# Kernel tuning notes

Hardware: AMD Instinct MI355X
Metric: run time of the kernel (lower is better)

## Reference

```python
import jax, jax.numpy as jnp
import numpy as np

D_MODEL = 1024
NUM_HEADS = 16
HEAD_DIM = D_MODEL // NUM_HEADS
NUM_KERNELS = 21


def tisa_bias(amp, off, sharp, seq_len):
    # amp/off/sharp: (H, K). Returns (H, L, L) translation-invariant bias.
    # Evaluate on the 2L-1 distinct relative distances, then gather (Toeplitz).
    d = jnp.arange(-(seq_len - 1), seq_len, dtype=amp.dtype)  # (2L-1,)
    # (H, K, 2L-1) -> sum over kernels -> (H, 2L-1)
    scores = jnp.sum(
        amp[:, :, None]
        * jnp.exp(-jnp.abs(sharp)[:, :, None] * (d[None, None, :] - off[:, :, None]) ** 2),
        axis=1,
    )
    i = jnp.arange(seq_len)
    rel_idx = i[None, :] - i[:, None] + (seq_len - 1)  # (L, L) in [0, 2L-2]
    return scores[:, rel_idx]  # (H, L, L)


def setup_inputs() -> dict:
    key = jax.random.key(0)
    ks = jax.random.split(key, 9)
    B, L = 4, 1024
    s = 0.02
    return {
        "x_q": jax.random.normal(ks[0], (B, L, D_MODEL), dtype=jnp.float32),
        "x_kv": jax.random.normal(ks[1], (B, L, D_MODEL), dtype=jnp.float32),
        "Wq": jax.random.normal(ks[2], (D_MODEL, D_MODEL), dtype=jnp.float32) * s,
        "Wm": jax.random.normal(ks[3], (D_MODEL, 2 * D_MODEL), dtype=jnp.float32) * s,
        "Wg": jax.random.normal(ks[4], (D_MODEL, 2 * D_MODEL), dtype=jnp.float32) * s,
        "bg": jnp.zeros((2 * D_MODEL,), dtype=jnp.float32),
        "tisa_amp": jax.random.normal(ks[5], (NUM_HEADS, NUM_KERNELS), dtype=jnp.float32) * 0.1,
        "tisa_off": jax.random.uniform(ks[6], (NUM_HEADS, NUM_KERNELS), dtype=jnp.float32, minval=-512.0, maxval=512.0),
        "tisa_sharp": jax.random.uniform(ks[7], (NUM_HEADS, NUM_KERNELS), dtype=jnp.float32, minval=1e-4, maxval=0.05),
    }


def reference(x_q, x_kv, Wq, Wm, Wg, bg, tisa_amp, tisa_off, tisa_sharp):
    B, Lq, _ = x_q.shape
    Lkv = x_kv.shape[1]
    H, Dh = NUM_HEADS, HEAD_DIM

    q = (x_q @ Wq).reshape(B, Lq, H, Dh).transpose(0, 2, 1, 3)        # (B,H,Lq,Dh)
    mem = (x_kv @ Wm)                                                 # (B,Lkv,2D)
    k = mem[..., :D_MODEL].reshape(B, Lkv, H, Dh).transpose(0, 2, 1, 3)
    v = mem[..., D_MODEL:].reshape(B, Lkv, H, Dh).transpose(0, 2, 1, 3)

    scale = 1.0 / jnp.sqrt(jnp.asarray(Dh, dtype=q.dtype))
    scores = jnp.einsum("bhqd,bhkd->bhqk", q, k) * scale              # (B,H,Lq,Lkv)
    scores = scores + tisa_bias(tisa_amp, tisa_off, tisa_sharp, Lkv)[None]
    weights = jax.nn.softmax(scores, axis=-1)

    attn = jnp.einsum("bhqk,bhkd->bhqd", weights, v)                  # (B,H,Lq,Dh)
    attn = attn.transpose(0, 2, 1, 3).reshape(B, Lq, D_MODEL)

    g = attn @ Wg + bg                                                # (B,Lq,2D)
    a, b = g[..., :D_MODEL], g[..., D_MODEL:]
    return a * jax.nn.sigmoid(b)
```

## Files before the change

### kernel.cpp

```cpp
#include <hip/hip_runtime.h>
#include <cstdint>
#include <cstddef>

typedef __attribute__((ext_vector_type(8))) short bf16x8;
typedef __attribute__((ext_vector_type(4))) float f32x4;

#define LOG2E 1.44269504f

__device__ __forceinline__ unsigned short f2bf(float x) {
  unsigned int u = __float_as_uint(x);
  u += 0x7FFFu + ((u >> 16) & 1u);
  return (unsigned short)(u >> 16);
}
__device__ __forceinline__ unsigned short f2bf_trunc(float x) {
  return (unsigned short)(__float_as_uint(x) >> 16);
}

__device__ __forceinline__ bf16x8 pack8(const float4& a, const float4& b) {
  bf16x8 r;
  r[0] = (short)f2bf(a.x); r[1] = (short)f2bf(a.y);
  r[2] = (short)f2bf(a.z); r[3] = (short)f2bf(a.w);
  r[4] = (short)f2bf(b.x); r[5] = (short)f2bf(b.y);
  r[6] = (short)f2bf(b.z); r[7] = (short)f2bf(b.w);
  return r;
}

__device__ __forceinline__ void gload_lds16(const void* g, void* l) {
  __builtin_amdgcn_global_load_lds(
      (const __attribute__((address_space(1))) unsigned int*)g,
      (__attribute__((address_space(3))) unsigned int*)l, 16, 0, 0);
}


__global__ void preproc(const float* __restrict__ Wq, const float* __restrict__ Wm,
                        const float* __restrict__ Wg,
                        const float* __restrict__ amp, const float* __restrict__ off,
                        const float* __restrict__ sharp,
                        unsigned short* __restrict__ dWq, unsigned short* __restrict__ dWm,
                        unsigned short* __restrict__ dWg, float* __restrict__ tab) {
  __shared__ float tile[32][33];
  const int blk = blockIdx.x;
  if (blk < 6144) {
    int idx = blk;
    int z = idx >> 11, rem = idx & 2047;
    int bx = rem & 63, by = rem >> 6;
    const float* src = z == 0 ? Wq : (z == 1 ? Wm : Wg);
    unsigned short* dst = z == 0 ? dWq : (z == 1 ? dWm : dWg);
    int N = z == 0 ? 1024 : 2048;
    int nb = bx * 32, kb = by * 32;
    if (nb >= N) return;
    int tx = threadIdx.x & 31, ty = threadIdx.x >> 5;
#pragma unroll
    for (int r = ty; r < 32; r += 8)
      tile[r][tx] = src[(size_t)(kb + r) * N + nb + tx];
    __syncthreads();
#pragma unroll
    for (int r = ty; r < 32; r += 8)
      dst[(size_t)(nb + r) * 1024 + kb + tx] = f2bf(tile[tx][r]);
  } else {
    int h = blk - 6144;
    for (int idx = threadIdx.x; idx < 2047; idx += 256) {
      float d = (float)(idx - 1023);
      float acc = 0.f;
#pragma unroll
      for (int k = 0; k < 21; ++k) {
        float dd = d - off[h * 21 + k];
        acc += amp[h * 21 + k] * __expf(-fabsf(sharp[h * 21 + k]) * dd * dd);
      }
      tab[h * 2047 + idx] = acc * LOG2E;
    }
  }
}


template <int MODE>
__global__ __launch_bounds__(256, 3)
void qkv128(const float* __restrict__ X, const unsigned short* __restrict__ WT,
            unsigned short* __restrict__ qbuf, unsigned short* __restrict__ kbuf,
            unsigned short* __restrict__ vtbuf) {
  __shared__ unsigned short sA[3][128 * 32];
  __shared__ unsigned short sB[3][128 * 32];
  const int ntile = blockIdx.y << 7;
  const int mtile = blockIdx.x << 7;
  const int t = threadIdx.x, lane = t & 63, w = t >> 6;
  const int wm = w >> 1, wn = w & 1;
  const int c = lane & 15, g = lane >> 4;

  const int sr = t >> 2;
  const int sch = (t & 3) ^ ((sr >> 1) & 3);
  const float* aP0 = X + (size_t)(mtile + sr) * 1024 + sch * 8;
  const float* aP1 = aP0 + 64 * 1024;
  const unsigned short* bP0 = WT + (size_t)(ntile + sr) * 1024 + sch * 8;
  const unsigned short* bP1 = bP0 + 64 * 1024;
  const int lw = t * 8;

  float4 pA[4], iA[4];
  bf16x8 pB[2], iB[2];
  {
    float4 c0 = *(const float4*)(aP0);
    float4 c1 = *(const float4*)(aP0 + 4);
    float4 c2 = *(const float4*)(aP1);
    float4 c3 = *(const float4*)(aP1 + 4);
    bf16x8 cB0 = *(const bf16x8*)(bP0);
    bf16x8 cB1 = *(const bf16x8*)(bP1);
    pA[0] = *(const float4*)(aP0 + 32);
    pA[1] = *(const float4*)(aP0 + 36);
    pA[2] = *(const float4*)(aP1 + 32);
    pA[3] = *(const float4*)(aP1 + 36);
    pB[0] = *(const bf16x8*)(bP0 + 32);
    pB[1] = *(const bf16x8*)(bP1 + 32);
    *(bf16x8*)&sA[0][lw]        = pack8(c0, c1);
    *(bf16x8*)&sA[0][2048 + lw] = pack8(c2, c3);
    *(bf16x8*)&sB[0][lw]        = cB0;
    *(bf16x8*)&sB[0][2048 + lw] = cB1;
  }
  asm volatile("s_waitcnt lgkmcnt(0)" ::: "memory");
  __builtin_amdgcn_sched_barrier(0);
  asm volatile("s_barrier" ::: "memory");

  const int gx = (g ^ ((c >> 1) & 3)) * 8;
  const int aoff = (wm * 64 + c) * 32 + gx;
  const int boff = (wn * 64 + c) * 32 + gx;

  f32x4 acc[4][4] = {};
  int s0 = 0, s1 = 1, s2 = 2;

  for (int kt = 0; kt < 32; ++kt) {
    if (kt + 2 < 32) {
      const int ko = (kt + 2) * 32;
      iA[0] = *(const float4*)(aP0 + ko);
      iA[1] = *(const float4*)(aP0 + ko + 4);
      iA[2] = *(const float4*)(aP1 + ko);
      iA[3] = *(const float4*)(aP1 + ko + 4);
      iB[0] = *(const bf16x8*)(bP0 + ko);
      iB[1] = *(const bf16x8*)(bP1 + ko);
    }

    const unsigned short* sAp = &sA[s0][0];
    const unsigned short* sBc = &sB[s0][0];
    bf16x8 af[4], bfr[4];
#pragma unroll
    for (int i = 0; i < 4; ++i) af[i]  = *(const bf16x8*)&sAp[aoff + i * 512];
#pragma unroll
    for (int j = 0; j < 4; ++j) bfr[j] = *(const bf16x8*)&sBc[boff + j * 512];

    __builtin_amdgcn_s_setprio(1);
#pragma unroll
    for (int i = 0; i < 4; ++i)
#pragma unroll
      for (int j = 0; j < 4; ++j)
        acc[i][j] = __builtin_amdgcn_mfma_f32_16x16x32_bf16(af[i], bfr[j], acc[i][j], 0, 0, 0);
    __builtin_amdgcn_s_setprio(0);

    if (kt + 1 < 32) {
      *(bf16x8*)&sA[s1][lw]        = pack8(pA[0], pA[1]);
      *(bf16x8*)&sA[s1][2048 + lw] = pack8(pA[2], pA[3]);
      *(bf16x8*)&sB[s1][lw]        = pB[0];
      *(bf16x8*)&sB[s1][2048 + lw] = pB[1];
    }
#pragma unroll
    for (int q = 0; q < 4; ++q) pA[q] = iA[q];
    pB[0] = iB[0]; pB[1] = iB[1];

    asm volatile("s_waitcnt lgkmcnt(0)" ::: "memory");
    __builtin_amdgcn_sched_barrier(0);
    asm volatile("s_barrier" ::: "memory");
    __builtin_amdgcn_sched_barrier(0);

    int tmp = s0; s0 = s1; s1 = s2; s2 = tmp;
  }

  const int row0 = mtile + wm * 64 + (g << 2);
  const int col0 = ntile + wn * 64 + c;
  if (MODE == 0) {
#pragma unroll
    for (int i = 0; i < 4; ++i)
#pragma unroll
      for (int j = 0; j < 4; ++j) {
        int r = row0 + i * 16, cl = col0 + j * 16;
#pragma unroll
        for (int ri = 0; ri < 4; ++ri)
          qbuf[(size_t)(r + ri) * 1024 + cl] = f2bf(acc[i][j][ri] * (0.125f * LOG2E));
      }
  } else if (ntile < 1024) {
#pragma unroll
    for (int i = 0; i < 4; ++i)
#pragma unroll
      for (int j = 0; j < 4; ++j) {
        int r = row0 + i * 16, cl = col0 + j * 16;
#pragma unroll
        for (int ri = 0; ri < 4; ++ri)
          kbuf[(size_t)(r + ri) * 1024 + cl] = f2bf(acc[i][j][ri]);
      }
  } else {
#pragma unroll
    for (int i = 0; i < 4; ++i)
#pragma unroll
      for (int j = 0; j < 4; ++j) {
        int r = row0 + i * 16, cl = col0 + j * 16;
        int d = cl - 1024;
        int hh = d >> 6, dh = d & 63;
        int bb2 = r >> 10, ll = r & 1023;
        ushort4 pk;
        pk.x = f2bf(acc[i][j][0]);
        pk.y = f2bf(acc[i][j][1]);
        pk.z = f2bf(acc[i][j][2]);
        pk.w = f2bf(acc[i][j][3]);
        *(ushort4*)&vtbuf[((size_t)((bb2 * 16 + hh) * 64 + dh) << 10) + ll] = pk;
      }
  }
}


__global__ __launch_bounds__(512)
void attn_kernel(const unsigned short* __restrict__ qbuf,
                 const unsigned short* __restrict__ kbuf,
                 const unsigned short* __restrict__ vtbuf,
                 const float* __restrict__ biasTab,
                 unsigned short* __restrict__ attnb) {
  const int h = blockIdx.x & 15, b = blockIdx.x >> 4, qt = blockIdx.y;
  __shared__ unsigned short sK[2][64 * 64];
  __shared__ unsigned short sV[3][64 * 64];
  __shared__ unsigned short sP[2][128 * 64];
  __shared__ float sLsum[2][128];
  const int t = threadIdx.x, lane = t & 63, w = t >> 6;
  const int c = lane & 15, g = lane >> 4;
  const int rg = w >> 1, cg = w & 1;

  const int r = t >> 3, ch = (t & 7) ^ (r & 7);

  const unsigned short* qsrc = qbuf + (size_t)(b * 1024 + qt * 128) * 1024 + h * 64;
  const unsigned short* ksrc = kbuf + (size_t)(b * 1024) * 1024 + h * 64;
  const unsigned short* vsrc = vtbuf + (size_t)((b * 16 + h) * 64) * 1024;

  unsigned short* sQ = &sP[0][0];
  gload_lds16(qsrc + (size_t)r * 1024 + ch * 8, &sQ[t * 8]);
  gload_lds16(qsrc + (size_t)(r + 64) * 1024 + ch * 8, &sQ[4096 + t * 8]);
  gload_lds16(ksrc + (size_t)r * 1024 + ch * 8, &sK[0][t * 8]);
  gload_lds16(vsrc + (size_t)r * 1024 + ch * 8, &sV[0][t * 8]);

  const float* bb = biasTab + h * 2047 + 1023 + cg * 32 + c - qt * 128 - rg * 32 - g * 4;

  float bc[2][2][4];
#pragma unroll
  for (int rf = 0; rf < 2; ++rf)
#pragma unroll
    for (int nf = 0; nf < 2; ++nf)
#pragma unroll
      for (int ri = 0; ri < 4; ++ri)
        bc[rf][nf][ri] = bb[(nf - rf) * 16 - ri];

  __syncthreads();

  bf16x8 aq[2][2];
#pragma unroll
  for (int rf = 0; rf < 2; ++rf) {
    int row = rg * 32 + rf * 16 + c;
#pragma unroll
    for (int ks = 0; ks < 2; ++ks)
      aq[rf][ks] = *(const bf16x8*)&sQ[row * 64 + (((ks * 4 + g) ^ (row & 7)) * 8)];
  }
  __syncthreads();

  f32x4 o[2][2] = {};
  float lsum[2][4] = {};

  int vcur = 0, vnx = 1;
  for (int kv = 0; kv < 16; ++kv) {
    const int cur = kv & 1;

    f32x4 s[2][2];
#pragma unroll
    for (int rf = 0; rf < 2; ++rf)
#pragma unroll
      for (int nf = 0; nf < 2; ++nf)
#pragma unroll
        for (int ri = 0; ri < 4; ++ri)
          s[rf][nf][ri] = bc[rf][nf][ri];

    if (kv + 1 < 16) {
      gload_lds16(ksrc + (size_t)((kv + 1) * 64 + r) * 1024 + ch * 8, &sK[1 - cur][t * 8]);
      gload_lds16(vsrc + (size_t)r * 1024 + (kv + 1) * 64 + ch * 8, &sV[vnx][t * 8]);
      const float* bk = bb + (kv + 1) * 64;
#pragma unroll
      for (int rf = 0; rf < 2; ++rf)
#pragma unroll
        for (int nf = 0; nf < 2; ++nf)
#pragma unroll
          for (int ri = 0; ri < 4; ++ri)
            bc[rf][nf][ri] = bk[(nf - rf) * 16 - ri];
    }

#pragma unroll
    for (int nf = 0; nf < 2; ++nf) {
      int krow = cg * 32 + nf * 16 + c;
      bf16x8 k0 = *(const bf16x8*)&sK[cur][krow * 64 + (((g) ^ (krow & 7)) * 8)];
      bf16x8 k1 = *(const bf16x8*)&sK[cur][krow * 64 + (((4 + g) ^ (krow & 7)) * 8)];
#pragma unroll
      for (int rf = 0; rf < 2; ++rf) {
        s[rf][nf] = __builtin_amdgcn_mfma_f32_16x16x32_bf16(aq[rf][0], k0, s[rf][nf], 0, 0, 0);
        s[rf][nf] = __builtin_amdgcn_mfma_f32_16x16x32_bf16(aq[rf][1], k1, s[rf][nf], 0, 0, 0);
      }
    }

#pragma unroll
    for (int rf = 0; rf < 2; ++rf)
#pragma unroll
      for (int nf = 0; nf < 2; ++nf)
#pragma unroll
        for (int ri = 0; ri < 4; ++ri) {
          float e = exp2f(s[rf][nf][ri]);
          lsum[rf][ri] += e;
          int prow = rg * 32 + rf * 16 + g * 4 + ri;
          int chunk = cg * 4 + nf * 2 + (c >> 3);
          sP[cur][prow * 64 + ((chunk ^ (prow & 7)) * 8) + (c & 7)] = f2bf_trunc(e);
        }
    __syncthreads();

    bf16x8 ap[2][2];
#pragma unroll
    for (int rf = 0; rf < 2; ++rf) {
      int row = rg * 32 + rf * 16 + c;
#pragma unroll
      for (int ks = 0; ks < 2; ++ks)
        ap[rf][ks] = *(const bf16x8*)&sP[cur][row * 64 + (((ks * 4 + g) ^ (row & 7)) * 8)];
    }
#pragma unroll
    for (int df = 0; df < 2; ++df) {
      int vrow = cg * 32 + df * 16 + c;
      bf16x8 v0 = *(const bf16x8*)&sV[vcur][vrow * 64 + (((g) ^ (vrow & 7)) * 8)];
      bf16x8 v1 = *(const bf16x8*)&sV[vcur][vrow * 64 + (((4 + g) ^ (vrow & 7)) * 8)];
#pragma unroll
      for (int rf = 0; rf < 2; ++rf) {
        o[rf][df] = __builtin_amdgcn_mfma_f32_16x16x32_bf16(ap[rf][0], v0, o[rf][df], 0, 0, 0);
        o[rf][df] = __builtin_amdgcn_mfma_f32_16x16x32_bf16(ap[rf][1], v1, o[rf][df], 0, 0, 0);
      }
    }
    vcur = vnx;
    vnx = (vnx == 2) ? 0 : vnx + 1;
  }

#pragma unroll
  for (int off = 1; off < 16; off <<= 1)
#pragma unroll
    for (int rf = 0; rf < 2; ++rf)
#pragma unroll
      for (int ri = 0; ri < 4; ++ri)
        lsum[rf][ri] += __shfl_xor(lsum[rf][ri], off, 64);
  if (c == 0) {
#pragma unroll
    for (int rf = 0; rf < 2; ++rf)
#pragma unroll
      for (int ri = 0; ri < 4; ++ri)
        sLsum[cg][rg * 32 + rf * 16 + g * 4 + ri] = lsum[rf][ri];
  }
  __syncthreads();

  unsigned short* obase = attnb +
      (size_t)(b * 1024 + qt * 128 + rg * 32 + g * 4) * 1024 + h * 64 + cg * 32 + c;
#pragma unroll
  for (int rf = 0; rf < 2; ++rf)
#pragma unroll
    for (int ri = 0; ri < 4; ++ri) {
      int row = rg * 32 + rf * 16 + g * 4 + ri;
      float rinv = 1.0f / (sLsum[0][row] + sLsum[1][row]);
#pragma unroll
      for (int df = 0; df < 2; ++df)
        obase[(size_t)(rf * 16 + ri) * 1024 + df * 16] = f2bf(o[rf][df][ri] * rinv);
    }
}


__global__ __launch_bounds__(256, 4)
void out_gemm(const unsigned short* __restrict__ A,
              const unsigned short* __restrict__ WgT,
              const float* __restrict__ bg,
              float* __restrict__ out) {
  __shared__ unsigned short sA[2][64 * 32];
  __shared__ unsigned short sB[2][128 * 32];
  const int nb = blockIdx.y;
  const int mtile = blockIdx.x << 6;
  const int t = threadIdx.x, lane = t & 63, w = t >> 6;
  const int c = lane & 15, g = lane >> 4;
  const int rm = w >> 1, cn = w & 1;
  const int srow = t >> 2, scol = (t & 3) << 3;
  const unsigned short* aP = A + (size_t)(mtile + srow) * 1024 + scol;
  const unsigned short* bP0 = WgT + (size_t)(nb * 64 + srow) * 1024 + scol;
  const unsigned short* bP1 = WgT + (size_t)(1024 + nb * 64 + srow) * 1024 + scol;
  const int lo = srow * 32 + scol;

  gload_lds16(aP, &sA[0][lo]);
  gload_lds16(bP0, &sB[0][lo]);
  gload_lds16(bP1, &sB[0][lo + 64 * 32]);
  __syncthreads();

  f32x4 acc[2][4] = {};
  for (int kt = 0; kt < 32; ++kt) {
    const int cur = kt & 1;
    if (kt + 1 < 32) {
      const int ko = (kt + 1) * 32;
      gload_lds16(aP + ko, &sA[1 - cur][lo]);
      gload_lds16(bP0 + ko, &sB[1 - cur][lo]);
      gload_lds16(bP1 + ko, &sB[1 - cur][lo + 64 * 32]);
    }
    bf16x8 af[2], bfr[4];
#pragma unroll
    for (int i = 0; i < 2; ++i)
      af[i] = *(const bf16x8*)&sA[cur][(rm * 32 + i * 16 + c) * 32 + g * 8];
#pragma unroll
    for (int jj = 0; jj < 2; ++jj) {
      bfr[jj]     = *(const bf16x8*)&sB[cur][(cn * 32 + jj * 16 + c) * 32 + g * 8];
      bfr[jj + 2] = *(const bf16x8*)&sB[cur][(64 + cn * 32 + jj * 16 + c) * 32 + g * 8];
    }
#pragma unroll
    for (int i = 0; i < 2; ++i)
#pragma unroll
      for (int j = 0; j < 4; ++j)
        acc[i][j] = __builtin_amdgcn_mfma_f32_16x16x32_bf16(af[i], bfr[j], acc[i][j], 0, 0, 0);
    __syncthreads();
  }

#pragma unroll
  for (int i = 0; i < 2; ++i) {
    int row0 = mtile + rm * 32 + i * 16 + (g << 2);
#pragma unroll
    for (int jj = 0; jj < 2; ++jj) {
      int col = nb * 64 + cn * 32 + jj * 16 + c;
      float ba = bg[col];
      float bbv = bg[1024 + col];
#pragma unroll
      for (int ri = 0; ri < 4; ++ri) {
        float av = acc[i][jj][ri] + ba;
        float bv = acc[i][jj + 2][ri] + bbv;
        out[(size_t)(row0 + ri) * 1024 + col] = av / (1.f + exp2f(-LOG2E * bv));
      }
    }
  }
}


extern "C" void kernel_launch(void* const* d_in, const int* in_sizes, int n_in,
                              void* d_out, int out_size, void* d_ws, size_t ws_size,
                              hipStream_t stream) {
  const float* x_q   = (const float*)d_in[0];
  const float* x_kv  = (const float*)d_in[1];
  const float* Wq    = (const float*)d_in[2];
  const float* Wm    = (const float*)d_in[3];
  const float* Wg    = (const float*)d_in[4];
  const float* bg    = (const float*)d_in[5];
  const float* amp   = (const float*)d_in[6];
  const float* off   = (const float*)d_in[7];
  const float* sharp = (const float*)d_in[8];
  float* out = (float*)d_out;

  char* ws = (char*)d_ws;
  size_t o = 0;
  auto alloc = [&](size_t bytes) {
    char* p = ws + o;
    o += (bytes + 255) & ~(size_t)255;
    return p;
  };
  unsigned short* bWqT  = (unsigned short*)alloc(1024ull * 1024 * 2);
  unsigned short* bWmT  = (unsigned short*)alloc(2048ull * 1024 * 2);
  unsigned short* bWgT  = (unsigned short*)alloc(2048ull * 1024 * 2);
  float*          biasT = (float*)alloc(16ull * 2047 * 4);
  unsigned short* qbuf  = (unsigned short*)alloc(4096ull * 1024 * 2);
  unsigned short* kbuf  = (unsigned short*)alloc(4096ull * 1024 * 2);
  unsigned short* vtbuf = (unsigned short*)alloc(4096ull * 1024 * 2);
  unsigned short* attnb = (unsigned short*)alloc(4096ull * 1024 * 2);
  if (ws_size < o) return;

  preproc<<<6160, 256, 0, stream>>>(Wq, Wm, Wg, amp, off, sharp,
                                    bWqT, bWmT, bWgT, biasT);
  qkv128<0><<<dim3(32, 8), 256, 0, stream>>>(x_q, bWqT, qbuf, nullptr, nullptr);
  qkv128<1><<<dim3(32, 16), 256, 0, stream>>>(x_kv, bWmT, nullptr, kbuf, vtbuf);
  attn_kernel<<<dim3(64, 8), 512, 0, stream>>>(qbuf, kbuf, vtbuf, biasT, attnb);
  out_gemm<<<dim3(64, 16), 256, 0, stream>>>(attnb, bWgT, bg, out);
}
```

Before: 220.3 us.

## Fuse weight preprocessing into QKV GEMM, reading fp32 weights directly

The separate transpose/convert pass over Wq and Wm is removed. The QKV GEMM now loads fp32 weight columns directly, converts them to bf16 and stores them into a swizzled LDS layout. The remaining preprocessing work (Wg transpose and the bias table) and the Q and KV GEMMs are merged into one launch, which saves kernel launches and a round trip through memory for the weight copies. In exchange, the B loads become strided scalar fp32 reads with double the bytes, 16 extra registers are held for prefetch, and the launch-bounds occupancy hint is dropped.

```diff
diff --git a/kernel.cpp b/kernel.cpp
--- a/kernel.cpp
+++ b/kernel.cpp
@@ -25,6 +25,13 @@
   return r;
 }
 
+__device__ __forceinline__ bf16x8 packcol(const float* v) {
+  bf16x8 r;
+#pragma unroll
+  for (int j = 0; j < 8; ++j) r[j] = (short)f2bf(v[j]);
+  return r;
+}
+
 __device__ __forceinline__ void gload_lds16(const void* g, void* l) {
   __builtin_amdgcn_global_load_lds(
       (const __attribute__((address_space(1))) unsigned int*)g,
@@ -32,57 +39,62 @@
 }
 
 
-__global__ void preproc(const float* __restrict__ Wq, const float* __restrict__ Wm,
-                        const float* __restrict__ Wg,
-                        const float* __restrict__ amp, const float* __restrict__ off,
-                        const float* __restrict__ sharp,
-                        unsigned short* __restrict__ dWq, unsigned short* __restrict__ dWm,
-                        unsigned short* __restrict__ dWg, float* __restrict__ tab) {
-  __shared__ float tile[32][33];
-  const int blk = blockIdx.x;
-  if (blk < 6144) {
-    int idx = blk;
-    int z = idx >> 11, rem = idx & 2047;
-    int bx = rem & 63, by = rem >> 6;
-    const float* src = z == 0 ? Wq : (z == 1 ? Wm : Wg);
-    unsigned short* dst = z == 0 ? dWq : (z == 1 ? dWm : dWg);
-    int N = z == 0 ? 1024 : 2048;
-    int nb = bx * 32, kb = by * 32;
-    if (nb >= N) return;
-    int tx = threadIdx.x & 31, ty = threadIdx.x >> 5;
-#pragma unroll
-    for (int r = ty; r < 32; r += 8)
-      tile[r][tx] = src[(size_t)(kb + r) * N + nb + tx];
-    __syncthreads();
-#pragma unroll
-    for (int r = ty; r < 32; r += 8)
-      dst[(size_t)(nb + r) * 1024 + kb + tx] = f2bf(tile[tx][r]);
-  } else {
-    int h = blk - 6144;
-    for (int idx = threadIdx.x; idx < 2047; idx += 256) {
-      float d = (float)(idx - 1023);
-      float acc = 0.f;
-#pragma unroll
-      for (int k = 0; k < 21; ++k) {
-        float dd = d - off[h * 21 + k];
-        acc += amp[h * 21 + k] * __expf(-fabsf(sharp[h * 21 + k]) * dd * dd);
-      }
-      tab[h * 2047 + idx] = acc * LOG2E;
-    }
-  }
-}
-
-
-template <int MODE>
-__global__ __launch_bounds__(256, 3)
-void qkv128(const float* __restrict__ X, const unsigned short* __restrict__ WT,
-            unsigned short* __restrict__ qbuf, unsigned short* __restrict__ kbuf,
-            unsigned short* __restrict__ vtbuf) {
-  __shared__ unsigned short sA[3][128 * 32];
-  __shared__ unsigned short sB[3][128 * 32];
-  const int ntile = blockIdx.y << 7;
-  const int mtile = blockIdx.x << 7;
-  const int t = threadIdx.x, lane = t & 63, w = t >> 6;
+__global__ __launch_bounds__(256)
+void qkv_direct(const float* __restrict__ x_q, const float* __restrict__ x_kv,
+                const float* __restrict__ Wq, const float* __restrict__ Wm,
+                const float* __restrict__ Wg,
+                const float* __restrict__ amp, const float* __restrict__ off,
+                const float* __restrict__ sharp,
+                unsigned short* __restrict__ bWgT, float* __restrict__ biasT,
+                unsigned short* __restrict__ qbuf, unsigned short* __restrict__ kbuf,
+                unsigned short* __restrict__ vtbuf) {
+  __shared__ __align__(16) char smem[49152];
+  const int bid = blockIdx.x;
+  const int t = threadIdx.x;
+
+  if (bid >= 768) {
+    if (bid < 2816) {
+      float* tile = (float*)smem;
+      const int idx = bid - 768;
+      const int bx = idx & 63, by = idx >> 6;
+      const int nb = bx * 32, kb = by * 32;
+      const int tx = t & 31, ty = t >> 5;
+#pragma unroll
+      for (int r = ty; r < 32; r += 8)
+        tile[r * 33 + tx] = Wg[(size_t)(kb + r) * 2048 + nb + tx];
+      __syncthreads();
+#pragma unroll
+      for (int r = ty; r < 32; r += 8)
+        bWgT[(size_t)(nb + r) * 1024 + kb + tx] = f2bf(tile[tx * 33 + r]);
+    } else {
+      const int h = bid - 2816;
+      for (int idx = t; idx < 2047; idx += 256) {
+        float d = (float)(idx - 1023);
+        float acc = 0.f;
+#pragma unroll
+        for (int k = 0; k < 21; ++k) {
+          float dd = d - off[h * 21 + k];
+          acc += amp[h * 21 + k] * __expf(-fabsf(sharp[h * 21 + k]) * dd * dd);
+        }
+        biasT[h * 2047 + idx] = acc * LOG2E;
+      }
+    }
+    return;
+  }
+
+  unsigned short* sA = (unsigned short*)smem;
+  unsigned short* sB = (unsigned short*)(smem + 24576);
+  const int jid = bid;
+  const bool isQ = jid < 256;
+  const int jr = isQ ? jid : jid - 256;
+  const int mt = jr & 31;
+  const int nt = jr >> 5;
+  const int mtile = mt << 7, ntile = nt << 7;
+  const float* X = isQ ? x_q : x_kv;
+  const float* W = isQ ? Wq : Wm;
+  const int N = isQ ? 1024 : 2048;
+
+  const int lane = t & 63, w = t >> 6;
   const int wm = w >> 1, wn = w & 1;
   const int c = lane & 15, g = lane >> 4;
 
@@ -90,40 +102,46 @@
   const int sch = (t & 3) ^ ((sr >> 1) & 3);
   const float* aP0 = X + (size_t)(mtile + sr) * 1024 + sch * 8;
   const float* aP1 = aP0 + 64 * 1024;
-  const unsigned short* bP0 = WT + (size_t)(ntile + sr) * 1024 + sch * 8;
-  const unsigned short* bP1 = bP0 + 64 * 1024;
   const int lw = t * 8;
 
+  const int bn = t & 127, bkg = t >> 7;
+  const float* bP = W + (size_t)(bkg * 16) * N + ntile + bn;
+  const int bkey = ((bn >> 1) & 3) ^ (((bn >> 3) & 1) << 1) ^ ((bn >> 4) & 3);
+  const int bw0 = bn * 32 + (((bkg * 2) ^ bkey) * 8);
+  const int bw1 = bn * 32 + (((bkg * 2 + 1) ^ bkey) * 8);
+
   float4 pA[4], iA[4];
-  bf16x8 pB[2], iB[2];
+  float pBv[16], iBv[16];
   {
     float4 c0 = *(const float4*)(aP0);
     float4 c1 = *(const float4*)(aP0 + 4);
     float4 c2 = *(const float4*)(aP1);
     float4 c3 = *(const float4*)(aP1 + 4);
-    bf16x8 cB0 = *(const bf16x8*)(bP0);
-    bf16x8 cB1 = *(const bf16x8*)(bP1);
+    float cb[16];
+#pragma unroll
+    for (int i = 0; i < 16; ++i) cb[i] = bP[(size_t)i * N];
     pA[0] = *(const float4*)(aP0 + 32);
     pA[1] = *(const float4*)(aP0 + 36);
     pA[2] = *(const float4*)(aP1 + 32);
     pA[3] = *(const float4*)(aP1 + 36);
-    pB[0] = *(const bf16x8*)(bP0 + 32);
-    pB[1] = *(const bf16x8*)(bP1 + 32);
-    *(bf16x8*)&sA[0][lw]        = pack8(c0, c1);
-    *(bf16x8*)&sA[0][2048 + lw] = pack8(c2, c3);
-    *(bf16x8*)&sB[0][lw]        = cB0;
-    *(bf16x8*)&sB[0][2048 + lw] = cB1;
+#pragma unroll
+    for (int i = 0; i < 16; ++i) pBv[i] = bP[(size_t)(32 + i) * N];
+    *(bf16x8*)&sA[lw]        = pack8(c0, c1);
+    *(bf16x8*)&sA[2048 + lw] = pack8(c2, c3);
+    *(bf16x8*)&sB[bw0] = packcol(cb);
+    *(bf16x8*)&sB[bw1] = packcol(cb + 8);
   }
   asm volatile("s_waitcnt lgkmcnt(0)" ::: "memory");
   __builtin_amdgcn_sched_barrier(0);
   asm volatile("s_barrier" ::: "memory");
 
-  const int gx = (g ^ ((c >> 1) & 3)) * 8;
-  const int aoff = (wm * 64 + c) * 32 + gx;
-  const int boff = (wn * 64 + c) * 32 + gx;
+  const int gxA = (g ^ ((c >> 1) & 3)) * 8;
+  const int aoff = (wm * 64 + c) * 32 + gxA;
+  const int kbse = ((c >> 1) & 3) ^ ((c >> 3) << 1);
+  const int brow = (wn * 64 + c) * 32;
 
   f32x4 acc[4][4] = {};
-  int s0 = 0, s1 = 1, s2 = 2;
+  int s0 = 0, s1 = 4096, s2 = 8192;
 
   for (int kt = 0; kt < 32; ++kt) {
     if (kt + 2 < 32) {
@@ -132,17 +150,18 @@
       iA[1] = *(const float4*)(aP0 + ko + 4);
       iA[2] = *(const float4*)(aP1 + ko);
       iA[3] = *(const float4*)(aP1 + ko + 4);
-      iB[0] = *(const bf16x8*)(bP0 + ko);
-      iB[1] = *(const bf16x8*)(bP1 + ko);
-    }
-
-    const unsigned short* sAp = &sA[s0][0];
-    const unsigned short* sBc = &sB[s0][0];
+#pragma unroll
+      for (int i = 0; i < 16; ++i) iBv[i] = bP[(size_t)(ko + i) * N];
+    }
+
+    const unsigned short* sAp = &sA[s0];
+    const unsigned short* sBc = &sB[s0];
     bf16x8 af[4], bfr[4];
 #pragma unroll
-    for (int i = 0; i < 4; ++i) af[i]  = *(const bf16x8*)&sAp[aoff + i * 512];
-#pragma unroll
-    for (int j = 0; j < 4; ++j) bfr[j] = *(const bf16x8*)&sBc[boff + j * 512];
+    for (int i = 0; i < 4; ++i) af[i] = *(const bf16x8*)&sAp[aoff + i * 512];
+#pragma unroll
+    for (int jj = 0; jj < 4; ++jj)
+      bfr[jj] = *(const bf16x8*)&sBc[brow + jj * 512 + ((g ^ kbse ^ jj) * 8)];
 
     __builtin_amdgcn_s_setprio(1);
 #pragma unroll
@@ -153,14 +172,15 @@
     __builtin_amdgcn_s_setprio(0);
 
     if (kt + 1 < 32) {
-      *(bf16x8*)&sA[s1][lw]        = pack8(pA[0], pA[1]);
-      *(bf16x8*)&sA[s1][2048 + lw] = pack8(pA[2], pA[3]);
-      *(bf16x8*)&sB[s1][lw]        = pB[0];
-      *(bf16x8*)&sB[s1][2048 + lw] = pB[1];
+      *(bf16x8*)&sA[s1 + lw]        = pack8(pA[0], pA[1]);
+      *(bf16x8*)&sA[s1 + 2048 + lw] = pack8(pA[2], pA[3]);
+      *(bf16x8*)&sB[s1 + bw0] = packcol(pBv);
+      *(bf16x8*)&sB[s1 + bw1] = packcol(pBv + 8);
     }
 #pragma unroll
     for (int q = 0; q < 4; ++q) pA[q] = iA[q];
-    pB[0] = iB[0]; pB[1] = iB[1];
+#pragma unroll
+    for (int q = 0; q < 16; ++q) pBv[q] = iBv[q];
 
     asm volatile("s_waitcnt lgkmcnt(0)" ::: "memory");
     __builtin_amdgcn_sched_barrier(0);
@@ -172,7 +192,7 @@
 
   const int row0 = mtile + wm * 64 + (g << 2);
   const int col0 = ntile + wn * 64 + c;
-  if (MODE == 0) {
+  if (isQ) {
 #pragma unroll
     for (int i = 0; i < 4; ++i)
 #pragma unroll
@@ -460,8 +480,6 @@
     o += (bytes + 255) & ~(size_t)255;
     return p;
   };
-  unsigned short* bWqT  = (unsigned short*)alloc(1024ull * 1024 * 2);
-  unsigned short* bWmT  = (unsigned short*)alloc(2048ull * 1024 * 2);
   unsigned short* bWgT  = (unsigned short*)alloc(2048ull * 1024 * 2);
   float*          biasT = (float*)alloc(16ull * 2047 * 4);
   unsigned short* qbuf  = (unsigned short*)alloc(4096ull * 1024 * 2);
@@ -470,10 +488,8 @@
   unsigned short* attnb = (unsigned short*)alloc(4096ull * 1024 * 2);
   if (ws_size < o) return;
 
-  preproc<<<6160, 256, 0, stream>>>(Wq, Wm, Wg, amp, off, sharp,
-                                    bWqT, bWmT, bWgT, biasT);
-  qkv128<0><<<dim3(32, 8), 256, 0, stream>>>(x_q, bWqT, qbuf, nullptr, nullptr);
-  qkv128<1><<<dim3(32, 16), 256, 0, stream>>>(x_kv, bWmT, nullptr, kbuf, vtbuf);
+  qkv_direct<<<2832, 256, 0, stream>>>(x_q, x_kv, Wq, Wm, Wg, amp, off, sharp,
+                                       bWgT, biasT, qbuf, kbuf, vtbuf);
   attn_kernel<<<dim3(64, 8), 512, 0, stream>>>(qbuf, kbuf, vtbuf, biasT, attnb);
   out_gemm<<<dim3(64, 16), 256, 0, stream>>>(attnb, bWgT, bg, out);
 }
```

After: 234.7 us. 6.5% more time.
